# Kernel tuning notes

Measured on AMD Instinct MI355X. Metric: run time of the kernel, lower is better.

Reference implementation:

```python
import jax, jax.numpy as jnp
import numpy as np

EMBED = 256      # hp.embed_size
ATT = 256        # hp.attention_size
KSZ = 5          # hp.kernel_size
L = 4            # hp.decoder_layers
N_MELS = 80
R = 4
KEY_PR = (4096 // 4) / 512.0   # hp.max_frames // hp.r / hp.max_timesteps = 2.0
QUERY_PR = 1.0
SQRT_HALF = float(np.sqrt(0.5))


def _pos_enc(T, C, pos_rate):
    # Faithful to source: angle_rates = pos*pos_rate/10000^(2*(k//2)/C); pe = pos*angle_rates
    pos = jnp.arange(T, dtype=jnp.float32)[:, None]            # [T,1]
    k = jnp.arange(C)[None, :]                                  # [1,C]
    power = jnp.power(jnp.float32(10000.0), 2.0 * (k // 2).astype(jnp.float32) / C)
    angle = pos * (pos * pos_rate / power)                      # [T,C]
    return jnp.where(k % 2 == 0, jnp.sin(angle), jnp.cos(angle))[None]  # [1,T,C]


def _conv_block(x, w, b, dilation):
    # causal dilated Conv1D + GLU + scaled residual. x:[B,T,C], w:[K,C,2C]
    pad = (KSZ - 1) * dilation
    y = jax.lax.conv_general_dilated(
        x, w, window_strides=(1,), padding=[(pad, 0)], rhs_dilation=(dilation,),
        dimension_numbers=('NWC', 'WIO', 'NWC')) + b
    a, g = jnp.split(y, 2, axis=-1)
    return (x + a * jax.nn.sigmoid(g)) * SQRT_HALF


def _attention(x, keys, values, w1, b1, w2, b2, w3, b3, wo, bo):
    Tq, Tk, C = x.shape[1], keys.shape[1], x.shape[-1]
    q = x + _pos_enc(Tq, C, QUERY_PR)
    k = keys + _pos_enc(Tk, C, KEY_PR)
    k_out = k @ w1 + b1           # fc1(keys)
    q_out = q @ w2 + b2           # fc2(query)
    v_out = values @ w3 + b3      # fc3(values)
    aw = jnp.einsum('bqd,bkd->bqk', q_out, k_out)
    # key_masks = ones_like(sum(keys_out,-1)) -> never zero, masking is a no-op (kept faithful)
    al = jax.nn.softmax(aw, axis=-1)  # dropout disabled (training=False)
    ctx = jnp.einsum('bqk,bkd->bqd', al, v_out) * jax.lax.rsqrt(jnp.float32(Tk))
    return ctx @ wo + bo


def setup_inputs() -> dict:
    key = jax.random.key(0)
    ks = jax.random.split(key, 16)
    s = jnp.float32(0.02)
    B, TQ, TK = 32, 1024, 512
    d = {}
    d['inputs'] = jax.random.normal(ks[0], (B, TQ, N_MELS * R), jnp.float32)
    d['keys'] = jax.random.normal(ks[1], (B, TK, EMBED), jnp.float32)
    d['values'] = jax.random.normal(ks[2], (B, TK, EMBED), jnp.float32)
    d['w_first'] = jax.random.normal(ks[3], (N_MELS * R, EMBED), jnp.float32) * s
    d['b_first'] = jnp.zeros((EMBED,), jnp.float32)
    d['fc_w'] = jax.random.normal(ks[4], (L - 1, EMBED, EMBED), jnp.float32) * s
    d['fc_b'] = jnp.zeros((L - 1, EMBED), jnp.float32)
    d['conv_w'] = jax.random.normal(ks[5], (L, KSZ, EMBED, 2 * EMBED), jnp.float32) * s
    d['conv_b'] = jnp.zeros((L, 2 * EMBED), jnp.float32)
    d['att_w1'] = jax.random.normal(ks[6], (L, EMBED, ATT), jnp.float32) * s
    d['att_b1'] = jnp.zeros((L, ATT), jnp.float32)
    d['att_w2'] = jax.random.normal(ks[7], (L, EMBED, ATT), jnp.float32) * s
    d['att_b2'] = jnp.zeros((L, ATT), jnp.float32)
    d['att_w3'] = jax.random.normal(ks[8], (L, EMBED, ATT), jnp.float32) * s
    d['att_b3'] = jnp.zeros((L, ATT), jnp.float32)
    d['att_wo'] = jax.random.normal(ks[9], (L, ATT, EMBED), jnp.float32) * s
    d['att_bo'] = jnp.zeros((L, EMBED), jnp.float32)
    d['w_done'] = jax.random.normal(ks[10], (EMBED, 2), jnp.float32) * s
    d['b_done'] = jnp.zeros((2,), jnp.float32)
    d['w_mel'] = jax.random.normal(ks[11], (EMBED, N_MELS * R), jnp.float32) * s
    d['b_mel'] = jnp.zeros((N_MELS * R,), jnp.float32)
    return d


def reference(inputs, keys, values, w_first, b_first, fc_w, fc_b, conv_w, conv_b,
              att_w1, att_b1, att_w2, att_b2, att_w3, att_b3, att_wo, att_bo,
              w_done, b_done, w_mel, b_mel):
    h = jax.nn.relu(inputs @ w_first + b_first)
    for i in range(L - 1):
        h = jax.nn.relu(h @ fc_w[i] + fc_b[i])
    for i in range(L):
        h = _conv_block(h, conv_w[i], conv_b[i], 2 ** i)
        att = _attention(h, keys, values,
                         att_w1[i], att_b1[i], att_w2[i], att_b2[i],
                         att_w3[i], att_b3[i], att_wo[i], att_bo[i])
        h = (att + h) * SQRT_HALF
    done_output = jax.nn.sigmoid(h @ w_done + b_done)
    mel_output = h @ w_mel + b_mel
    return (mel_output, done_output, h)
```

## Files before the change

kernel.cpp:

```cpp
#include <hip/hip_runtime.h>
#include <hip/hip_bf16.h>
#include <math.h>

#define SQH 0.70710678118654752440f

typedef __bf16 bf16x8 __attribute__((ext_vector_type(8)));
typedef float f32x4 __attribute__((ext_vector_type(4)));

__device__ __forceinline__ void glds16(const void* g, void* l) {
    __builtin_amdgcn_global_load_lds((const __attribute__((address_space(1))) void*)g,
                                     (__attribute__((address_space(3))) void*)l, 16, 0, 0);
}

__global__ void pos_enc_kernel(float* __restrict__ pe, int T, float rate) {
    int idx = blockIdx.x * blockDim.x + threadIdx.x;
    if (idx >= T * 256) return;
    int t = idx >> 8;
    int k = idx & 255;
    float e = 2.0f * (float)(k >> 1) / 256.0f;
    float pw = powf(10000.0f, e);
    float ang = (float)t * ((float)t * rate / pw);
    pe[idx] = ((k & 1) == 0) ? sinf(ang) : cosf(ang);
}

__global__ void zero_init(float* z) { z[threadIdx.x] = 0.f; }

__global__ __launch_bounds__(256) void cvt_bf(const float* __restrict__ src,
                                              __bf16* __restrict__ dst, long n8) {
    long i = (long)blockIdx.x * 256 + threadIdx.x;
    if (i >= n8) return;
    const float* s = src + i * 8;
    float4 a = *(const float4*)s, b = *(const float4*)(s + 4);
    bf16x8 o;
    o[0] = (__bf16)a.x; o[1] = (__bf16)a.y; o[2] = (__bf16)a.z; o[3] = (__bf16)a.w;
    o[4] = (__bf16)b.x; o[5] = (__bf16)b.y; o[6] = (__bf16)b.z; o[7] = (__bf16)b.w;
    *(bf16x8*)(dst + i * 8) = o;
}

__global__ __launch_bounds__(256) void kpe_kernel(const float* __restrict__ keys,
                                                  const float* __restrict__ pek,
                                                  __bf16* __restrict__ dst) {
    long i = (long)blockIdx.x * 256 + threadIdx.x;
    long row = i >> 5; int c8 = (int)(i & 31) << 3;
    const float* kp = keys + row * 256 + c8;
    const float* pp = pek + (row & 511) * 256 + c8;
    float4 a = *(const float4*)kp, b = *(const float4*)(kp + 4);
    float4 p = *(const float4*)pp, q = *(const float4*)(pp + 4);
    bf16x8 o;
    o[0] = (__bf16)(a.x + p.x); o[1] = (__bf16)(a.y + p.y);
    o[2] = (__bf16)(a.z + p.z); o[3] = (__bf16)(a.w + p.w);
    o[4] = (__bf16)(b.x + q.x); o[5] = (__bf16)(b.y + q.y);
    o[6] = (__bf16)(b.z + q.z); o[7] = (__bf16)(b.w + q.w);
    *(bf16x8*)(dst + i * 8) = o;
}

__global__ __launch_bounds__(256) void transpose_k(const float* __restrict__ src,
                                                   __bf16* __restrict__ dst,
                                                   int R, int Cc, long sS, long sD) {
    __shared__ float tile[32][33];
    src += (long)blockIdx.z * sS;
    dst += (long)blockIdx.z * sD;
    int c0 = blockIdx.x * 32, r0 = blockIdx.y * 32;
    int tx = threadIdx.x & 31, ty = threadIdx.x >> 5;
#pragma unroll
    for (int p = 0; p < 4; ++p)
        tile[ty + 8 * p][tx] = src[(long)(r0 + ty + 8 * p) * Cc + c0 + tx];
    __syncthreads();
#pragma unroll
    for (int p = 0; p < 4; ++p)
        dst[(long)(c0 + ty + 8 * p) * R + r0 + tx] = (__bf16)tile[tx][ty + 8 * p];
}

template<int BIAS_MODE, int ACT, int OUT_MODE, int RES>
__global__ __launch_bounds__(256) void gemm_bf(
    const __bf16* __restrict__ A, const __bf16* __restrict__ Bt,
    const float* __restrict__ bias, const float* __restrict__ res,
    float* __restrict__ outF, __bf16* __restrict__ outB,
    int M, int N, int K, long sA, long sB, long sC)
{
    __shared__ __align__(16) __bf16 As[4096];
    __shared__ __align__(16) __bf16 Bs[4096];
    const int z = blockIdx.z;
    A += (long)z * sA;
    Bt += (long)z * sB;
    const int row0 = blockIdx.y << 7, col0 = blockIdx.x << 7;
    const int tid = threadIdx.x, wid = tid >> 6, lane = tid & 63;
    const int lrow = lane & 15, lkp = lane >> 4;
    const int wm = (wid >> 1) << 6, wn = (wid & 1) << 6;
    const int srow = (wid << 5) + (lane >> 2);
    const int kq8 = (lane & 3) << 3;
    const __bf16* Ap0 = A + (long)(row0 + srow) * K + kq8;
    const __bf16* Ap1 = Ap0 + (long)16 * K;
    int c0i = col0 + srow, c1i = col0 + srow + 16;
    if (c0i > N - 1) c0i = N - 1;
    if (c1i > N - 1) c1i = N - 1;
    const __bf16* Bp0 = Bt + (long)c0i * K + kq8;
    const __bf16* Bp1 = Bt + (long)c1i * K + kq8;
    __bf16* AsW = As + (wid << 10);
    __bf16* BsW = Bs + (wid << 10);

    f32x4 acc[4][4];
#pragma unroll
    for (int i = 0; i < 4; ++i)
#pragma unroll
        for (int j = 0; j < 4; ++j) acc[i][j] = (f32x4){0.f, 0.f, 0.f, 0.f};

    for (int k0 = 0; k0 < K; k0 += 32) {
        glds16(Ap0 + k0, AsW);
        glds16(Ap1 + k0, AsW + 512);
        glds16(Bp0 + k0, BsW);
        glds16(Bp1 + k0, BsW + 512);
        __syncthreads();
        bf16x8 af[4], bfr[4];
        const __bf16* Ar = As + (wm + lrow) * 32 + lkp * 8;
        const __bf16* Br = Bs + (wn + lrow) * 32 + lkp * 8;
#pragma unroll
        for (int i = 0; i < 4; ++i) af[i] = *(const bf16x8*)(Ar + i * 512);
#pragma unroll
        for (int j = 0; j < 4; ++j) bfr[j] = *(const bf16x8*)(Br + j * 512);
#pragma unroll
        for (int i = 0; i < 4; ++i)
#pragma unroll
            for (int j = 0; j < 4; ++j)
                acc[i][j] = __builtin_amdgcn_mfma_f32_16x16x32_bf16(af[i], bfr[j], acc[i][j], 0, 0, 0);
        __syncthreads();
    }

    float* oF = outF ? outF + (long)z * sC : nullptr;
    __bf16* oB = outB ? outB + (long)z * sC : nullptr;
    const float* resp = RES ? res + (long)z * sC : nullptr;
#pragma unroll
    for (int i = 0; i < 4; ++i) {
#pragma unroll
        for (int r = 0; r < 4; ++r) {
            const int gr = row0 + wm + i * 16 + lkp * 4 + r;
#pragma unroll
            for (int j = 0; j < 4; ++j) {
                const int gc = col0 + wn + j * 16 + lrow;
                if (gc >= N) continue;
                float v = acc[i][j][r];
                if (BIAS_MODE == 1) v += bias[gc];
                if (BIAS_MODE == 2) v += bias[gr];
                if (RES) v = (v + resp[(long)gr * N + gc]) * SQH;
                if (ACT == 1) v = fmaxf(v, 0.f);
                if (OUT_MODE == 0 || OUT_MODE == 2) oF[(long)gr * N + gc] = v;
                if (OUT_MODE == 1 || OUT_MODE == 2) oB[(long)gr * N + gc] = (__bf16)v;
            }
        }
    }
}

__global__ __launch_bounds__(256) void conv_bf(
    const __bf16* __restrict__ hbf, const __bf16* __restrict__ Wt,
    const float* __restrict__ bias, __bf16* __restrict__ y, int dil,
    const __bf16* __restrict__ zp)
{
    __shared__ __align__(16) __bf16 As[4096];
    __shared__ __align__(16) __bf16 Bs[4096];
    const int row0 = blockIdx.y << 7, col0 = blockIdx.x << 7;
    const int tid = threadIdx.x, wid = tid >> 6, lane = tid & 63;
    const int lrow = lane & 15, lkp = lane >> 4;
    const int wm = (wid >> 1) << 6, wn = (wid & 1) << 6;
    const int srow = (wid << 5) + (lane >> 2);
    const int kq8 = (lane & 3) << 3;
    const int grow = row0 + srow;
    const int t0 = (row0 & 1023) + srow;
    const __bf16* Bp0 = Wt + (long)(col0 + srow) * 1280 + kq8;
    const __bf16* Bp1 = Bp0 + (long)16 * 1280;
    __bf16* AsW = As + (wid << 10);
    __bf16* BsW = Bs + (wid << 10);

    f32x4 acc[4][4];
#pragma unroll
    for (int i = 0; i < 4; ++i)
#pragma unroll
        for (int j = 0; j < 4; ++j) acc[i][j] = (f32x4){0.f, 0.f, 0.f, 0.f};

    for (int k0 = 0; k0 < 1280; k0 += 32) {
        const int tap = k0 >> 8;
        const int off = (4 - tap) * dil;
        const int kc = (k0 & 255) + kq8;
        const __bf16* a0 = (t0 >= off) ? hbf + (long)(grow - off) * 256 + kc : zp;
        const __bf16* a1 = (t0 + 16 >= off) ? hbf + (long)(grow + 16 - off) * 256 + kc : zp;
        glds16(a0, AsW);
        glds16(a1, AsW + 512);
        glds16(Bp0 + k0, BsW);
        glds16(Bp1 + k0, BsW + 512);
        __syncthreads();
        bf16x8 af[4], bfr[4];
        const __bf16* Ar = As + (wm + lrow) * 32 + lkp * 8;
        const __bf16* Br = Bs + (wn + lrow) * 32 + lkp * 8;
#pragma unroll
        for (int i = 0; i < 4; ++i) af[i] = *(const bf16x8*)(Ar + i * 512);
#pragma unroll
        for (int j = 0; j < 4; ++j) bfr[j] = *(const bf16x8*)(Br + j * 512);
#pragma unroll
        for (int i = 0; i < 4; ++i)
#pragma unroll
            for (int j = 0; j < 4; ++j)
                acc[i][j] = __builtin_amdgcn_mfma_f32_16x16x32_bf16(af[i], bfr[j], acc[i][j], 0, 0, 0);
        __syncthreads();
    }
#pragma unroll
    for (int i = 0; i < 4; ++i) {
#pragma unroll
        for (int r = 0; r < 4; ++r) {
            const int gr = row0 + wm + i * 16 + lkp * 4 + r;
#pragma unroll
            for (int j = 0; j < 4; ++j) {
                const int gc = col0 + wn + j * 16 + lrow;
                y[(long)gr * 512 + gc] = (__bf16)(acc[i][j][r] + bias[gc]);
            }
        }
    }
}

__global__ __launch_bounds__(256) void glu_kernel(float* __restrict__ h,
                                                  const __bf16* __restrict__ y,
                                                  const float* __restrict__ peq,
                                                  __bf16* __restrict__ h_bf,
                                                  __bf16* __restrict__ hq_bf) {
    long i = (long)blockIdx.x * 256 + threadIdx.x;
    long row = i >> 5; int c8 = (int)(i & 31) << 3;
    bf16x8 av = *(const bf16x8*)&y[row * 512 + c8];
    bf16x8 gv = *(const bf16x8*)&y[row * 512 + 256 + c8];
    float* hp = &h[row * 256 + c8];
    float4 h0 = *(float4*)hp, h1 = *(float4*)(hp + 4);
    const float* pp = &peq[(row & 1023) * 256 + c8];
    float4 p0 = *(const float4*)pp, p1 = *(const float4*)(pp + 4);
    float hv[8] = {h0.x, h0.y, h0.z, h0.w, h1.x, h1.y, h1.z, h1.w};
    float pv[8] = {p0.x, p0.y, p0.z, p0.w, p1.x, p1.y, p1.z, p1.w};
    float o[8];
    bf16x8 ob, oq;
#pragma unroll
    for (int q = 0; q < 8; ++q) {
        float a = (float)av[q], g = (float)gv[q];
        float v = (hv[q] + a / (1.f + expf(-g))) * SQH;
        o[q] = v;
        ob[q] = (__bf16)v;
        oq[q] = (__bf16)(v + pv[q]);
    }
    *(float4*)hp = make_float4(o[0], o[1], o[2], o[3]);
    *(float4*)(hp + 4) = make_float4(o[4], o[5], o[6], o[7]);
    *(bf16x8*)&h_bf[row * 256 + c8] = ob;
    *(bf16x8*)&hq_bf[row * 256 + c8] = oq;
}

__global__ __launch_bounds__(256) void softmax_bf(__bf16* __restrict__ aw) {
    int wv = threadIdx.x >> 6, lane = threadIdx.x & 63;
    long row = (long)blockIdx.x * 4 + wv;
    __bf16* p = aw + row * 512 + lane * 8;
    bf16x8 v = *(const bf16x8*)p;
    float f[8];
#pragma unroll
    for (int q = 0; q < 8; ++q) f[q] = (float)v[q];
    float m = f[0];
#pragma unroll
    for (int q = 1; q < 8; ++q) m = fmaxf(m, f[q]);
#pragma unroll
    for (int s = 32; s; s >>= 1) m = fmaxf(m, __shfl_xor(m, s));
    float sum = 0.f;
#pragma unroll
    for (int q = 0; q < 8; ++q) { f[q] = expf(f[q] - m); sum += f[q]; }
#pragma unroll
    for (int s = 32; s; s >>= 1) sum += __shfl_xor(sum, s);
    float sc = 0.04419417382415922f / sum;
#pragma unroll
    for (int q = 0; q < 8; ++q) v[q] = (__bf16)(f[q] * sc);
    *(bf16x8*)p = v;
}

__global__ __launch_bounds__(256) void done_kernel(const float* __restrict__ h,
                                                   const float* __restrict__ w,
                                                   const float* __restrict__ b,
                                                   float* __restrict__ out) {
    int row = blockIdx.x * 4 + (threadIdx.x >> 6);
    int lane = threadIdx.x & 63;
    float4 hv = *(const float4*)(h + (long)row * 256 + lane * 4);
    float4 w0 = *(const float4*)(w + lane * 8);
    float4 w1 = *(const float4*)(w + lane * 8 + 4);
    float d0 = hv.x * w0.x + hv.y * w0.z + hv.z * w1.x + hv.w * w1.z;
    float d1 = hv.x * w0.y + hv.y * w0.w + hv.z * w1.y + hv.w * w1.w;
#pragma unroll
    for (int s = 32; s; s >>= 1) { d0 += __shfl_xor(d0, s); d1 += __shfl_xor(d1, s); }
    if (lane == 0) {
        out[(long)row * 2 + 0] = 1.f / (1.f + expf(-(d0 + b[0])));
        out[(long)row * 2 + 1] = 1.f / (1.f + expf(-(d1 + b[1])));
    }
}

extern "C" void kernel_launch(void* const* d_in, const int* in_sizes, int n_in,
                              void* d_out, int out_size, void* d_ws, size_t ws_size,
                              hipStream_t stream) {
    const float* inputs  = (const float*)d_in[0];
    const float* keys    = (const float*)d_in[1];
    const float* values  = (const float*)d_in[2];
    const float* w_first = (const float*)d_in[3];
    const float* b_first = (const float*)d_in[4];
    const float* fc_w    = (const float*)d_in[5];
    const float* fc_b    = (const float*)d_in[6];
    const float* conv_w  = (const float*)d_in[7];
    const float* conv_b  = (const float*)d_in[8];
    const float* w1 = (const float*)d_in[9];  const float* b1 = (const float*)d_in[10];
    const float* w2 = (const float*)d_in[11]; const float* b2 = (const float*)d_in[12];
    const float* w3 = (const float*)d_in[13]; const float* b3 = (const float*)d_in[14];
    const float* wo = (const float*)d_in[15]; const float* bo = (const float*)d_in[16];
    const float* w_done = (const float*)d_in[17]; const float* b_done = (const float*)d_in[18];
    const float* w_mel  = (const float*)d_in[19]; const float* b_mel  = (const float*)d_in[20];
    float* out = (float*)d_out;
    float* ws  = (float*)d_ws;

    float* peq = ws;
    float* pek = peq + 262144;
    float* zp  = pek + 131072;
    float* h   = zp + 64;
    __bf16* bfb   = (__bf16*)(h + 8388608);
    __bf16* h_bf  = bfb;
    __bf16* hq_bf = h_bf  + 8388608;
    __bf16* y_bf  = hq_bf + 8388608;
    __bf16* q_bf  = y_bf  + 16777216;
    __bf16* k_bf  = q_bf  + 8388608;
    __bf16* kpe_bf= k_bf  + 4194304;
    __bf16* val_bf= kpe_bf+ 4194304;
    __bf16* vT_bf = val_bf+ 4194304;
    __bf16* awb   = vT_bf + 4194304;
    __bf16* ctx_bf= awb   + 16777216;
    __bf16* wfT   = ctx_bf+ 8388608;
    __bf16* fcT   = wfT   + 81920;
    __bf16* convT = fcT   + 196608;
    __bf16* w1T   = convT + 2621440;
    __bf16* w2T   = w1T   + 262144;
    __bf16* w3T   = w2T   + 262144;
    __bf16* woT   = w3T   + 262144;
    __bf16* wmT   = woT   + 262144;
    __bf16* in_bf = awb;

    dim3 blk(256);

    pos_enc_kernel<<<1024, 256, 0, stream>>>(peq, 1024, 1.0f);
    pos_enc_kernel<<<512, 256, 0, stream>>>(pek, 512, 2.0f);
    zero_init<<<1, 64, 0, stream>>>(zp);

    cvt_bf<<<5120, 256, 0, stream>>>(inputs, in_bf, 1310720);
    cvt_bf<<<2048, 256, 0, stream>>>(values, val_bf, 524288);
    kpe_kernel<<<2048, 256, 0, stream>>>(keys, pek, kpe_bf);

    transpose_k<<<dim3(8, 10, 1), blk, 0, stream>>>(w_first, wfT, 320, 256, 0, 0);
    transpose_k<<<dim3(8, 8, 3), blk, 0, stream>>>(fc_w, fcT, 256, 256, 65536, 65536);
    transpose_k<<<dim3(16, 40, 4), blk, 0, stream>>>(conv_w, convT, 1280, 512, 655360, 655360);
    transpose_k<<<dim3(8, 8, 4), blk, 0, stream>>>(w1, w1T, 256, 256, 65536, 65536);
    transpose_k<<<dim3(8, 8, 4), blk, 0, stream>>>(w2, w2T, 256, 256, 65536, 65536);
    transpose_k<<<dim3(8, 8, 4), blk, 0, stream>>>(w3, w3T, 256, 256, 65536, 65536);
    transpose_k<<<dim3(8, 8, 4), blk, 0, stream>>>(wo, woT, 256, 256, 65536, 65536);
    transpose_k<<<dim3(10, 8, 1), blk, 0, stream>>>(w_mel, wmT, 256, 320, 0, 0);

    gemm_bf<1, 1, 1, 0><<<dim3(2, 256, 1), blk, 0, stream>>>(
        in_bf, wfT, b_first, nullptr, nullptr, h_bf, 32768, 256, 320, 0, 0, 0);
    gemm_bf<1, 1, 1, 0><<<dim3(2, 256, 1), blk, 0, stream>>>(
        h_bf, fcT + 0 * 65536, fc_b + 0 * 256, nullptr, nullptr, hq_bf, 32768, 256, 256, 0, 0, 0);
    gemm_bf<1, 1, 1, 0><<<dim3(2, 256, 1), blk, 0, stream>>>(
        hq_bf, fcT + 1 * 65536, fc_b + 1 * 256, nullptr, nullptr, ctx_bf, 32768, 256, 256, 0, 0, 0);
    gemm_bf<1, 1, 2, 0><<<dim3(2, 256, 1), blk, 0, stream>>>(
        ctx_bf, fcT + 2 * 65536, fc_b + 2 * 256, nullptr, h, h_bf, 32768, 256, 256, 0, 0, 0);

    for (int l = 0; l < 4; ++l) {
        int dil = 1 << l;
        conv_bf<<<dim3(4, 256, 1), blk, 0, stream>>>(
            h_bf, convT + (long)l * 655360, conv_b + l * 512, y_bf, dil, (const __bf16*)zp);
        glu_kernel<<<4096, 256, 0, stream>>>(h, y_bf, peq, h_bf, hq_bf);
        gemm_bf<1, 0, 1, 0><<<dim3(2, 256, 1), blk, 0, stream>>>(
            hq_bf, w2T + (long)l * 65536, b2 + l * 256, nullptr, nullptr, q_bf, 32768, 256, 256, 0, 0, 0);
        gemm_bf<1, 0, 1, 0><<<dim3(2, 128, 1), blk, 0, stream>>>(
            kpe_bf, w1T + (long)l * 65536, b1 + l * 256, nullptr, nullptr, k_bf, 16384, 256, 256, 0, 0, 0);
        gemm_bf<2, 0, 1, 0><<<dim3(4, 2, 32), blk, 0, stream>>>(
            w3T + (long)l * 65536, val_bf, b3 + l * 256, nullptr, nullptr, vT_bf,
            256, 512, 256, 0, 512 * 256, 256 * 512);
        gemm_bf<0, 0, 1, 0><<<dim3(4, 8, 32), blk, 0, stream>>>(
            q_bf, k_bf, nullptr, nullptr, nullptr, awb,
            1024, 512, 256, 1024 * 256, 512 * 256, 1024 * 512);
        softmax_bf<<<8192, 256, 0, stream>>>(awb);
        gemm_bf<0, 0, 1, 0><<<dim3(2, 8, 32), blk, 0, stream>>>(
            awb, vT_bf, nullptr, nullptr, nullptr, ctx_bf,
            1024, 256, 512, 1024 * 512, 256 * 512, 1024 * 256);
        gemm_bf<1, 0, 2, 1><<<dim3(2, 256, 1), blk, 0, stream>>>(
            ctx_bf, woT + (long)l * 65536, bo + l * 256, h, h, h_bf, 32768, 256, 256, 0, 0, 0);
    }

    gemm_bf<1, 0, 0, 0><<<dim3(3, 256, 1), blk, 0, stream>>>(
        h_bf, wmT, b_mel, nullptr, out, nullptr, 32768, 320, 256, 0, 0, 0);
    done_kernel<<<8192, 256, 0, stream>>>(h, w_done, b_done, out + 10485760);
    hipMemcpyAsync(out + 10551296, h, (size_t)8388608 * 4, hipMemcpyDeviceToDevice, stream);
}
```

Baseline: 1.326 ms.

## Fuse conv with GLU epilogue, fuse scores with softmax, add XCD block swizzle

The conv kernel now computes the matching 'a' and 'gate' column tiles together and applies the GLU, residual and positional-encoding add in its epilogue. This removes the bf16 y intermediate and the separate GLU pass. The QK^T score GEMM and the softmax are merged into one 512-thread kernel, where each block owns 128 full key rows and reduces through shared memory, so the separate softmax read/write pass goes away. GEMM blocks are also remapped so adjacent tiles land on the same XCD. The costs are more accumulator registers (possible occupancy loss) and added ping-pong buffers for the fp32 and bf16 hidden state.

```diff
diff --git a/kernel.cpp b/kernel.cpp
--- a/kernel.cpp
+++ b/kernel.cpp
@@ -10,6 +10,11 @@
 __device__ __forceinline__ void glds16(const void* g, void* l) {
     __builtin_amdgcn_global_load_lds((const __attribute__((address_space(1))) void*)g,
                                      (__attribute__((address_space(3))) void*)l, 16, 0, 0);
+}
+
+__device__ __forceinline__ int xcd_swz(int lin, int n) {
+    if (n & 7) return lin;
+    return (lin & 7) * (n >> 3) + (lin >> 3);
 }
 
 __global__ void pos_enc_kernel(float* __restrict__ pe, int T, float rate) {
@@ -80,10 +85,13 @@
 {
     __shared__ __align__(16) __bf16 As[4096];
     __shared__ __align__(16) __bf16 Bs[4096];
-    const int z = blockIdx.z;
+    const int gx = gridDim.x, gy = gridDim.y;
+    int lin = (blockIdx.z * gy + blockIdx.y) * gx + blockIdx.x;
+    lin = xcd_swz(lin, gx * gy * gridDim.z);
+    const int bx = lin % gx, by = (lin / gx) % gy, z = lin / (gx * gy);
     A += (long)z * sA;
     Bt += (long)z * sB;
-    const int row0 = blockIdx.y << 7, col0 = blockIdx.x << 7;
+    const int row0 = by << 7, col0 = bx << 7;
     const int tid = threadIdx.x, wid = tid >> 6, lane = tid & 63;
     const int lrow = lane & 15, lkp = lane >> 4;
     const int wm = (wid >> 1) << 6, wn = (wid & 1) << 6;
@@ -150,14 +158,21 @@
     }
 }
 
-__global__ __launch_bounds__(256) void conv_bf(
-    const __bf16* __restrict__ hbf, const __bf16* __restrict__ Wt,
-    const float* __restrict__ bias, __bf16* __restrict__ y, int dil,
-    const __bf16* __restrict__ zp)
+__global__ __launch_bounds__(256) void conv_glu(
+    const __bf16* __restrict__ hbf, const float* __restrict__ hin,
+    const __bf16* __restrict__ Wt, const float* __restrict__ bias,
+    const float* __restrict__ peq,
+    float* __restrict__ hc_f, __bf16* __restrict__ hc_b, __bf16* __restrict__ hq_b,
+    int dil, const __bf16* __restrict__ zp)
 {
     __shared__ __align__(16) __bf16 As[4096];
-    __shared__ __align__(16) __bf16 Bs[4096];
-    const int row0 = blockIdx.y << 7, col0 = blockIdx.x << 7;
+    __shared__ __align__(16) __bf16 Ba[4096];
+    __shared__ __align__(16) __bf16 Bg[4096];
+    const int gx = gridDim.x;
+    int lin = blockIdx.y * gx + blockIdx.x;
+    lin = xcd_swz(lin, gx * gridDim.y);
+    const int bx = lin % gx, by = lin / gx;
+    const int row0 = by << 7, col0 = bx << 7;
     const int tid = threadIdx.x, wid = tid >> 6, lane = tid & 63;
     const int lrow = lane & 15, lkp = lane >> 4;
     const int wm = (wid >> 1) << 6, wn = (wid & 1) << 6;
@@ -165,16 +180,22 @@
     const int kq8 = (lane & 3) << 3;
     const int grow = row0 + srow;
     const int t0 = (row0 & 1023) + srow;
-    const __bf16* Bp0 = Wt + (long)(col0 + srow) * 1280 + kq8;
-    const __bf16* Bp1 = Bp0 + (long)16 * 1280;
+    const __bf16* Ba0 = Wt + (long)(col0 + srow) * 1280 + kq8;
+    const __bf16* Ba1 = Ba0 + (long)16 * 1280;
+    const __bf16* Bg0 = Wt + (long)(col0 + 256 + srow) * 1280 + kq8;
+    const __bf16* Bg1 = Bg0 + (long)16 * 1280;
     __bf16* AsW = As + (wid << 10);
-    __bf16* BsW = Bs + (wid << 10);
-
-    f32x4 acc[4][4];
-#pragma unroll
-    for (int i = 0; i < 4; ++i)
-#pragma unroll
-        for (int j = 0; j < 4; ++j) acc[i][j] = (f32x4){0.f, 0.f, 0.f, 0.f};
+    __bf16* BaW = Ba + (wid << 10);
+    __bf16* BgW = Bg + (wid << 10);
+
+    f32x4 aca[4][4], acg[4][4];
+#pragma unroll
+    for (int i = 0; i < 4; ++i)
+#pragma unroll
+        for (int j = 0; j < 4; ++j) {
+            aca[i][j] = (f32x4){0.f, 0.f, 0.f, 0.f};
+            acg[i][j] = (f32x4){0.f, 0.f, 0.f, 0.f};
+        }
 
     for (int k0 = 0; k0 < 1280; k0 += 32) {
         const int tap = k0 >> 8;
@@ -184,21 +205,26 @@
         const __bf16* a1 = (t0 + 16 >= off) ? hbf + (long)(grow + 16 - off) * 256 + kc : zp;
         glds16(a0, AsW);
         glds16(a1, AsW + 512);
-        glds16(Bp0 + k0, BsW);
-        glds16(Bp1 + k0, BsW + 512);
-        __syncthreads();
-        bf16x8 af[4], bfr[4];
+        glds16(Ba0 + k0, BaW);
+        glds16(Ba1 + k0, BaW + 512);
+        glds16(Bg0 + k0, BgW);
+        glds16(Bg1 + k0, BgW + 512);
+        __syncthreads();
+        bf16x8 af[4], ba[4], bg[4];
         const __bf16* Ar = As + (wm + lrow) * 32 + lkp * 8;
-        const __bf16* Br = Bs + (wn + lrow) * 32 + lkp * 8;
+        const __bf16* Bar = Ba + (wn + lrow) * 32 + lkp * 8;
+        const __bf16* Bgr = Bg + (wn + lrow) * 32 + lkp * 8;
 #pragma unroll
         for (int i = 0; i < 4; ++i) af[i] = *(const bf16x8*)(Ar + i * 512);
 #pragma unroll
-        for (int j = 0; j < 4; ++j) bfr[j] = *(const bf16x8*)(Br + j * 512);
+        for (int j = 0; j < 4; ++j) { ba[j] = *(const bf16x8*)(Bar + j * 512); bg[j] = *(const bf16x8*)(Bgr + j * 512); }
 #pragma unroll
         for (int i = 0; i < 4; ++i)
 #pragma unroll
-            for (int j = 0; j < 4; ++j)
-                acc[i][j] = __builtin_amdgcn_mfma_f32_16x16x32_bf16(af[i], bfr[j], acc[i][j], 0, 0, 0);
+            for (int j = 0; j < 4; ++j) {
+                aca[i][j] = __builtin_amdgcn_mfma_f32_16x16x32_bf16(af[i], ba[j], aca[i][j], 0, 0, 0);
+                acg[i][j] = __builtin_amdgcn_mfma_f32_16x16x32_bf16(af[i], bg[j], acg[i][j], 0, 0, 0);
+            }
         __syncthreads();
     }
 #pragma unroll
@@ -206,68 +232,129 @@
 #pragma unroll
         for (int r = 0; r < 4; ++r) {
             const int gr = row0 + wm + i * 16 + lkp * 4 + r;
+            const long rb = (long)gr * 256;
+            const long pb = (long)(gr & 1023) * 256;
 #pragma unroll
             for (int j = 0; j < 4; ++j) {
-                const int gc = col0 + wn + j * 16 + lrow;
-                y[(long)gr * 512 + gc] = (__bf16)(acc[i][j][r] + bias[gc]);
+                const int ca = col0 + wn + j * 16 + lrow;
+                float a = aca[i][j][r] + bias[ca];
+                float g = acg[i][j][r] + bias[ca + 256];
+                float v = (hin[rb + ca] + a / (1.f + expf(-g))) * SQH;
+                hc_f[rb + ca] = v;
+                hc_b[rb + ca] = (__bf16)v;
+                hq_b[rb + ca] = (__bf16)(v + peq[pb + ca]);
             }
         }
     }
 }
 
-__global__ __launch_bounds__(256) void glu_kernel(float* __restrict__ h,
-                                                  const __bf16* __restrict__ y,
-                                                  const float* __restrict__ peq,
-                                                  __bf16* __restrict__ h_bf,
-                                                  __bf16* __restrict__ hq_bf) {
-    long i = (long)blockIdx.x * 256 + threadIdx.x;
-    long row = i >> 5; int c8 = (int)(i & 31) << 3;
-    bf16x8 av = *(const bf16x8*)&y[row * 512 + c8];
-    bf16x8 gv = *(const bf16x8*)&y[row * 512 + 256 + c8];
-    float* hp = &h[row * 256 + c8];
-    float4 h0 = *(float4*)hp, h1 = *(float4*)(hp + 4);
-    const float* pp = &peq[(row & 1023) * 256 + c8];
-    float4 p0 = *(const float4*)pp, p1 = *(const float4*)(pp + 4);
-    float hv[8] = {h0.x, h0.y, h0.z, h0.w, h1.x, h1.y, h1.z, h1.w};
-    float pv[8] = {p0.x, p0.y, p0.z, p0.w, p1.x, p1.y, p1.z, p1.w};
-    float o[8];
-    bf16x8 ob, oq;
-#pragma unroll
-    for (int q = 0; q < 8; ++q) {
-        float a = (float)av[q], g = (float)gv[q];
-        float v = (hv[q] + a / (1.f + expf(-g))) * SQH;
-        o[q] = v;
-        ob[q] = (__bf16)v;
-        oq[q] = (__bf16)(v + pv[q]);
-    }
-    *(float4*)hp = make_float4(o[0], o[1], o[2], o[3]);
-    *(float4*)(hp + 4) = make_float4(o[4], o[5], o[6], o[7]);
-    *(bf16x8*)&h_bf[row * 256 + c8] = ob;
-    *(bf16x8*)&hq_bf[row * 256 + c8] = oq;
-}
-
-__global__ __launch_bounds__(256) void softmax_bf(__bf16* __restrict__ aw) {
-    int wv = threadIdx.x >> 6, lane = threadIdx.x & 63;
-    long row = (long)blockIdx.x * 4 + wv;
-    __bf16* p = aw + row * 512 + lane * 8;
-    bf16x8 v = *(const bf16x8*)p;
-    float f[8];
-#pragma unroll
-    for (int q = 0; q < 8; ++q) f[q] = (float)v[q];
-    float m = f[0];
-#pragma unroll
-    for (int q = 1; q < 8; ++q) m = fmaxf(m, f[q]);
-#pragma unroll
-    for (int s = 32; s; s >>= 1) m = fmaxf(m, __shfl_xor(m, s));
-    float sum = 0.f;
-#pragma unroll
-    for (int q = 0; q < 8; ++q) { f[q] = expf(f[q] - m); sum += f[q]; }
-#pragma unroll
-    for (int s = 32; s; s >>= 1) sum += __shfl_xor(sum, s);
-    float sc = 0.04419417382415922f / sum;
-#pragma unroll
-    for (int q = 0; q < 8; ++q) v[q] = (__bf16)(f[q] * sc);
-    *(bf16x8*)p = v;
+__global__ __launch_bounds__(512) void scores_sm(
+    const __bf16* __restrict__ Q, const __bf16* __restrict__ Kb,
+    __bf16* __restrict__ aw)
+{
+    __shared__ __align__(16) __bf16 As[128 * 32];
+    __shared__ __align__(16) __bf16 Bs[512 * 32];
+    __shared__ float redM[4][128];
+    __shared__ float redS[4][128];
+    int lin = xcd_swz(blockIdx.x, gridDim.x);
+    const int rt = lin & 7, z = lin >> 3;
+    const int row0 = rt << 7;
+    const __bf16* Az = Q + (long)z * 1024 * 256;
+    const __bf16* Bz = Kb + (long)z * 512 * 256;
+    __bf16* awz = aw + (long)z * 1024 * 512;
+    const int tid = threadIdx.x, wid = tid >> 6, lane = tid & 63;
+    const int lrow = lane & 15, lkp = lane >> 4;
+    const int wr = wid >> 2, wc = wid & 3;
+    const int sr = lane >> 2;
+    const int kq8 = (lane & 3) << 3;
+
+    f32x4 acc[4][8];
+#pragma unroll
+    for (int i = 0; i < 4; ++i)
+#pragma unroll
+        for (int j = 0; j < 8; ++j) acc[i][j] = (f32x4){0.f, 0.f, 0.f, 0.f};
+
+    for (int k0 = 0; k0 < 256; k0 += 32) {
+        glds16(Az + (long)(row0 + (wid << 4) + sr) * 256 + k0 + kq8, As + (wid << 9));
+#pragma unroll
+        for (int c = 0; c < 4; ++c) {
+            const int R = ((c << 3) + wid) << 4;
+            glds16(Bz + (long)(R + sr) * 256 + k0 + kq8, Bs + (R << 5));
+        }
+        __syncthreads();
+        bf16x8 af[4], bfr[8];
+        const __bf16* Ar = As + ((wr << 6) + lrow) * 32 + lkp * 8;
+        const __bf16* Br = Bs + ((wc << 7) + lrow) * 32 + lkp * 8;
+#pragma unroll
+        for (int i = 0; i < 4; ++i) af[i] = *(const bf16x8*)(Ar + i * 512);
+#pragma unroll
+        for (int j = 0; j < 8; ++j) bfr[j] = *(const bf16x8*)(Br + j * 512);
+#pragma unroll
+        for (int i = 0; i < 4; ++i)
+#pragma unroll
+            for (int j = 0; j < 8; ++j)
+                acc[i][j] = __builtin_amdgcn_mfma_f32_16x16x32_bf16(af[i], bfr[j], acc[i][j], 0, 0, 0);
+        __syncthreads();
+    }
+
+    float mx[4][4];
+#pragma unroll
+    for (int i = 0; i < 4; ++i)
+#pragma unroll
+        for (int r = 0; r < 4; ++r) {
+            float m = acc[i][0][r];
+#pragma unroll
+            for (int j = 1; j < 8; ++j) m = fmaxf(m, acc[i][j][r]);
+#pragma unroll
+            for (int s = 1; s < 16; s <<= 1) m = fmaxf(m, __shfl_xor(m, s));
+            mx[i][r] = m;
+        }
+    if (lrow == 0) {
+#pragma unroll
+        for (int i = 0; i < 4; ++i)
+#pragma unroll
+            for (int r = 0; r < 4; ++r)
+                redM[wc][(wr << 6) + i * 16 + (lkp << 2) + r] = mx[i][r];
+    }
+    __syncthreads();
+    float sm[4][4];
+#pragma unroll
+    for (int i = 0; i < 4; ++i)
+#pragma unroll
+        for (int r = 0; r < 4; ++r) {
+            const int row = (wr << 6) + i * 16 + (lkp << 2) + r;
+            float m = fmaxf(fmaxf(redM[0][row], redM[1][row]), fmaxf(redM[2][row], redM[3][row]));
+            float s = 0.f;
+#pragma unroll
+            for (int j = 0; j < 8; ++j) {
+                float p = expf(acc[i][j][r] - m);
+                acc[i][j][r] = p;
+                s += p;
+            }
+#pragma unroll
+            for (int sft = 1; sft < 16; sft <<= 1) s += __shfl_xor(s, sft);
+            sm[i][r] = s;
+        }
+    if (lrow == 0) {
+#pragma unroll
+        for (int i = 0; i < 4; ++i)
+#pragma unroll
+            for (int r = 0; r < 4; ++r)
+                redS[wc][(wr << 6) + i * 16 + (lkp << 2) + r] = sm[i][r];
+    }
+    __syncthreads();
+#pragma unroll
+    for (int i = 0; i < 4; ++i)
+#pragma unroll
+        for (int r = 0; r < 4; ++r) {
+            const int row = (wr << 6) + i * 16 + (lkp << 2) + r;
+            float S = redS[0][row] + redS[1][row] + redS[2][row] + redS[3][row];
+            float sc = 0.04419417382415922f / S;
+            __bf16* op = awz + (long)(row0 + row) * 512 + (wc << 7) + lrow;
+#pragma unroll
+            for (int j = 0; j < 8; ++j)
+                op[j * 16] = (__bf16)(acc[i][j][r] * sc);
+        }
 }
 
 __global__ __launch_bounds__(256) void done_kernel(const float* __restrict__ h,
@@ -310,22 +397,21 @@
     float* out = (float*)d_out;
     float* ws  = (float*)d_ws;
 
-    float* peq = ws;
-    float* pek = peq + 262144;
-    float* zp  = pek + 131072;
-    float* h   = zp + 64;
-    __bf16* bfb   = (__bf16*)(h + 8388608);
-    __bf16* h_bf  = bfb;
-    __bf16* hq_bf = h_bf  + 8388608;
-    __bf16* y_bf  = hq_bf + 8388608;
-    __bf16* q_bf  = y_bf  + 16777216;
+    float* peq  = ws;
+    float* pek  = peq + 262144;
+    float* zp   = pek + 131072;
+    float* h_f  = zp + 64;
+    float* hc_f = h_f + 8388608;
+    __bf16* h_b   = (__bf16*)(hc_f + 8388608);
+    __bf16* hc_b  = h_b   + 8388608;
+    __bf16* hq_b  = hc_b  + 8388608;
+    __bf16* q_bf  = hq_b  + 8388608;
     __bf16* k_bf  = q_bf  + 8388608;
     __bf16* kpe_bf= k_bf  + 4194304;
     __bf16* val_bf= kpe_bf+ 4194304;
     __bf16* vT_bf = val_bf+ 4194304;
     __bf16* awb   = vT_bf + 4194304;
-    __bf16* ctx_bf= awb   + 16777216;
-    __bf16* wfT   = ctx_bf+ 8388608;
+    __bf16* wfT   = awb   + 16777216;
     __bf16* fcT   = wfT   + 81920;
     __bf16* convT = fcT   + 196608;
     __bf16* w1T   = convT + 2621440;
@@ -334,6 +420,7 @@
     __bf16* woT   = w3T   + 262144;
     __bf16* wmT   = woT   + 262144;
     __bf16* in_bf = awb;
+    __bf16* ctx_bf = q_bf;
 
     dim3 blk(256);
 
@@ -355,39 +442,36 @@
     transpose_k<<<dim3(10, 8, 1), blk, 0, stream>>>(w_mel, wmT, 256, 320, 0, 0);
 
     gemm_bf<1, 1, 1, 0><<<dim3(2, 256, 1), blk, 0, stream>>>(
-        in_bf, wfT, b_first, nullptr, nullptr, h_bf, 32768, 256, 320, 0, 0, 0);
+        in_bf, wfT, b_first, nullptr, nullptr, h_b, 32768, 256, 320, 0, 0, 0);
     gemm_bf<1, 1, 1, 0><<<dim3(2, 256, 1), blk, 0, stream>>>(
-        h_bf, fcT + 0 * 65536, fc_b + 0 * 256, nullptr, nullptr, hq_bf, 32768, 256, 256, 0, 0, 0);
+        h_b, fcT + 0 * 65536, fc_b + 0 * 256, nullptr, nullptr, hq_b, 32768, 256, 256, 0, 0, 0);
     gemm_bf<1, 1, 1, 0><<<dim3(2, 256, 1), blk, 0, stream>>>(
-        hq_bf, fcT + 1 * 65536, fc_b + 1 * 256, nullptr, nullptr, ctx_bf, 32768, 256, 256, 0, 0, 0);
+        hq_b, fcT + 1 * 65536, fc_b + 1 * 256, nullptr, nullptr, hc_b, 32768, 256, 256, 0, 0, 0);
     gemm_bf<1, 1, 2, 0><<<dim3(2, 256, 1), blk, 0, stream>>>(
-        ctx_bf, fcT + 2 * 65536, fc_b + 2 * 256, nullptr, h, h_bf, 32768, 256, 256, 0, 0, 0);
+        hc_b, fcT + 2 * 65536, fc_b + 2 * 256, nullptr, h_f, h_b, 32768, 256, 256, 0, 0, 0);
 
     for (int l = 0; l < 4; ++l) {
         int dil = 1 << l;
-        conv_bf<<<dim3(4, 256, 1), blk, 0, stream>>>(
-            h_bf, convT + (long)l * 655360, conv_b + l * 512, y_bf, dil, (const __bf16*)zp);
-        glu_kernel<<<4096, 256, 0, stream>>>(h, y_bf, peq, h_bf, hq_bf);
+        conv_glu<<<dim3(2, 256, 1), blk, 0, stream>>>(
+            h_b, h_f, convT + (long)l * 655360, conv_b + l * 512, peq,
+            hc_f, hc_b, hq_b, dil, (const __bf16*)zp);
         gemm_bf<1, 0, 1, 0><<<dim3(2, 256, 1), blk, 0, stream>>>(
-            hq_bf, w2T + (long)l * 65536, b2 + l * 256, nullptr, nullptr, q_bf, 32768, 256, 256, 0, 0, 0);
+            hq_b, w2T + (long)l * 65536, b2 + l * 256, nullptr, nullptr, q_bf, 32768, 256, 256, 0, 0, 0);
         gemm_bf<1, 0, 1, 0><<<dim3(2, 128, 1), blk, 0, stream>>>(
             kpe_bf, w1T + (long)l * 65536, b1 + l * 256, nullptr, nullptr, k_bf, 16384, 256, 256, 0, 0, 0);
         gemm_bf<2, 0, 1, 0><<<dim3(4, 2, 32), blk, 0, stream>>>(
             w3T + (long)l * 65536, val_bf, b3 + l * 256, nullptr, nullptr, vT_bf,
             256, 512, 256, 0, 512 * 256, 256 * 512);
-        gemm_bf<0, 0, 1, 0><<<dim3(4, 8, 32), blk, 0, stream>>>(
-            q_bf, k_bf, nullptr, nullptr, nullptr, awb,
-            1024, 512, 256, 1024 * 256, 512 * 256, 1024 * 512);
-        softmax_bf<<<8192, 256, 0, stream>>>(awb);
+        scores_sm<<<256, 512, 0, stream>>>(q_bf, k_bf, awb);
         gemm_bf<0, 0, 1, 0><<<dim3(2, 8, 32), blk, 0, stream>>>(
             awb, vT_bf, nullptr, nullptr, nullptr, ctx_bf,
             1024, 256, 512, 1024 * 512, 256 * 512, 1024 * 256);
         gemm_bf<1, 0, 2, 1><<<dim3(2, 256, 1), blk, 0, stream>>>(
-            ctx_bf, woT + (long)l * 65536, bo + l * 256, h, h, h_bf, 32768, 256, 256, 0, 0, 0);
+            ctx_bf, woT + (long)l * 65536, bo + l * 256, hc_f, h_f, h_b, 32768, 256, 256, 0, 0, 0);
     }
 
     gemm_bf<1, 0, 0, 0><<<dim3(3, 256, 1), blk, 0, stream>>>(
-        h_bf, wmT, b_mel, nullptr, out, nullptr, 32768, 320, 256, 0, 0, 0);
-    done_kernel<<<8192, 256, 0, stream>>>(h, w_done, b_done, out + 10485760);
-    hipMemcpyAsync(out + 10551296, h, (size_t)8388608 * 4, hipMemcpyDeviceToDevice, stream);
-}
+        h_b, wmT, b_mel, nullptr, out, nullptr, 32768, 320, 256, 0, 0, 0);
+    done_kernel<<<8192, 256, 0, stream>>>(h_f, w_done, b_done, out + 10485760);
+    hipMemcpyAsync(out + 10551296, h_f, (size_t)8388608 * 4, hipMemcpyDeviceToDevice, stream);
+}
```

Result: no change. 1.336 ms (+0.8%).
